# Performance work log

Hardware: AMD Instinct MI355X
Metric: run time of the kernel (lower is better)

Reference implementation:

```python
import jax, jax.numpy as jnp
import numpy as np

B, S, H = 2, 2048, 1024
G, HEADS = 4, 16
HPG = HEADS // G          # heads per group = 4
HD = H // HEADS           # head_dim = 64
DG = H // G               # per-group proj dim = 256
SCALE = 1.0 / np.sqrt(HD)


def setup_inputs() -> dict:
    key = jax.random.key(0)
    ks = jax.random.split(key, 6)
    w = 0.02
    return {
        "hidden_states": jax.random.normal(ks[0], (B, S, H), dtype=jnp.float32),
        "Wq": jax.random.normal(ks[1], (G, DG, H), dtype=jnp.float32) * w,
        "bq": jnp.zeros((G, DG), dtype=jnp.float32),
        "Wk": jax.random.normal(ks[2], (G, DG, H), dtype=jnp.float32) * w,
        "bk": jnp.zeros((G, DG), dtype=jnp.float32),
        "Wv": jax.random.normal(ks[3], (G, DG, H), dtype=jnp.float32) * w,
        "bv": jnp.zeros((G, DG), dtype=jnp.float32),
        "Wo": jax.random.normal(ks[4], (H, H), dtype=jnp.float32) * w,
        "bo": jnp.zeros((H,), dtype=jnp.float32),
    }


def _proj_split(x, W, b):
    # x: [B,S,H], W: [G,DG,H], b: [G,DG] -> [B,G,HPG,S,HD]
    y = jnp.einsum("bsh,gdh->bgsd", x, W) + b[None, :, None, :]
    y = y.reshape(x.shape[0], G, x.shape[1], HPG, HD)
    return jnp.transpose(y, (0, 1, 3, 2, 4))


def reference(hidden_states, Wq, bq, Wk, bk, Wv, bv, Wo, bo):
    q = _proj_split(hidden_states, Wq, bq)  # [B,G,HPG,S,HD]
    k = _proj_split(hidden_states, Wk, bk)
    v = _proj_split(hidden_states, Wv, bv)
    scores = jnp.einsum("bghqd,bghkd->bghqk", q, k) * SCALE
    attn = jax.nn.softmax(scores.astype(jnp.float32), axis=-1).astype(v.dtype)
    ctx = jnp.einsum("bghqk,bghkd->bghqd", attn, v)  # [B,G,HPG,S,HD]
    # merge: heads ordered group-major, matching torch cat over group dim
    ctx = jnp.transpose(ctx, (0, 3, 1, 2, 4)).reshape(hidden_states.shape[0], hidden_states.shape[1], H)
    return jnp.einsum("bsh,oh->bso", ctx, Wo) + bo
```

## Files before the change

### kernel.cpp

```cpp
#include <hip/hip_runtime.h>

typedef __bf16 bf16x8 __attribute__((ext_vector_type(8)));
typedef __bf16 bf16x4 __attribute__((ext_vector_type(4)));
typedef short short4v __attribute__((ext_vector_type(4)));
typedef float f32x4 __attribute__((ext_vector_type(4)));

#define LOG2E 1.4426950408889634f

static __device__ __forceinline__ unsigned short f2bf(float f) {
  union { float f; unsigned int u; } c; c.f = f;
  return (unsigned short)((c.u + 0x7fffu + ((c.u >> 16) & 1u)) >> 16);
}

static __device__ __forceinline__ void gload16(const void* g, void* l) {
  __builtin_amdgcn_global_load_lds(
      (const __attribute__((address_space(1))) void*)g,
      (__attribute__((address_space(3))) void*)l, 16, 0, 0);
}

static __device__ __forceinline__ float expfast(float x) {
#if __has_builtin(__builtin_amdgcn_exp2f)
  return __builtin_amdgcn_exp2f(x * LOG2E);
#else
  return exp2f(x * LOG2E);
#endif
}

#if __has_builtin(__builtin_amdgcn_mfma_f32_16x16x16bf16_1k)
#define MFMA16_FALLBACK 0
static __device__ __forceinline__ f32x4 mfma16(bf16x4 a, bf16x4 b, f32x4 c) {
  return __builtin_amdgcn_mfma_f32_16x16x16bf16_1k(
      __builtin_bit_cast(short4v, a), __builtin_bit_cast(short4v, b), c, 0, 0, 0);
}
#else
#define MFMA16_FALLBACK 1
static __device__ __forceinline__ f32x4 mfma16(bf16x4 a, bf16x4 b, f32x4 c) {
  f32x4 d;
  asm("s_nop 1\n\tv_mfma_f32_16x16x16_bf16 %0, %1, %2, %3"
      : "=v"(d) : "v"(a), "v"(b), "v"(c));
  return d;
}
#endif

__global__ void cvt_all(const float* __restrict__ x,
                        const float* __restrict__ Wq,
                        const float* __restrict__ Wk,
                        const float* __restrict__ Wv,
                        const float* __restrict__ Wo,
                        ushort4* __restrict__ dst) {
  int i = blockIdx.x * 256 + threadIdx.x;
  const float* src;
  int off;
  if (i < 1048576) {
    src = x; off = i;
  } else {
    int t = (i - 1048576) >> 18;
    off = (i - 1048576) & 262143;
    src = (t == 0) ? Wq : (t == 1) ? Wk : (t == 2) ? Wv : Wo;
  }
  float4 f = ((const float4*)src)[off];
  ushort4 o;
  o.x = f2bf(f.x); o.y = f2bf(f.y); o.z = f2bf(f.z); o.w = f2bf(f.w);
  dst[i] = o;
}

__launch_bounds__(256, 2)
__global__ void qkv_gemm(const unsigned short* __restrict__ xb,
                         const unsigned short* __restrict__ wq,
                         const unsigned short* __restrict__ wk,
                         const unsigned short* __restrict__ wv,
                         const float* __restrict__ bq,
                         const float* __restrict__ bk,
                         const float* __restrict__ bv,
                         unsigned short* __restrict__ Qo,
                         unsigned short* __restrict__ Ko,
                         unsigned short* __restrict__ VTo) {
  __shared__ unsigned short As[128 * 64];
  __shared__ unsigned short Bs[128 * 64];
  const int s0 = blockIdx.x * 128;
  const int n0g = blockIdx.y * 128;
  const int qkv = n0g >> 10;
  const int d0 = n0g & 1023;
  const unsigned short* W = (qkv == 0) ? wq : ((qkv == 1) ? wk : wv);
  const float* bias = (qkv == 0) ? bq : ((qkv == 1) ? bk : bv);

  const unsigned short* Aptr; const unsigned short* Bptr;
  int Aoff, Boff;
  if (qkv < 2) { Aptr = W;  Aoff = d0; Bptr = xb; Boff = s0; }
  else         { Aptr = xb; Aoff = s0; Bptr = W;  Boff = d0; }

  const int tid = threadIdx.x;
  const int lane = tid & 63;
  const int wid = tid >> 6;
  const int wm = (wid >> 1) * 64;
  const int wn = (wid & 1) * 64;
  const int lm = lane & 15;
  const int quad = lane >> 4;

  f32x4 acc[4][4] = {};

  for (int kk = 0; kk < 1024; kk += 64) {
#pragma unroll
    for (int t = 0; t < 4; ++t) {
      int i = t * 256 + tid;
      int row = i >> 3, tp = i & 7;
      int seg = tp ^ (row & 7);
      gload16(Aptr + (size_t)(Aoff + row) * 1024 + kk + seg * 8,
              As + (size_t)i * 8);
      gload16(Bptr + (size_t)(Boff + row) * 1024 + kk + seg * 8,
              Bs + (size_t)i * 8);
    }
    __syncthreads();
#pragma unroll
    for (int h = 0; h < 2; ++h) {
      bf16x8 af[4], bff[4];
#pragma unroll
      for (int mt = 0; mt < 4; ++mt) {
        int r = wm + mt * 16 + lm;
        af[mt] = *(const bf16x8*)(As + r * 64 + (((h * 4 + quad) ^ (r & 7)) * 8));
      }
#pragma unroll
      for (int nt = 0; nt < 4; ++nt) {
        int r = wn + nt * 16 + lm;
        bff[nt] = *(const bf16x8*)(Bs + r * 64 + (((h * 4 + quad) ^ (r & 7)) * 8));
      }
#pragma unroll
      for (int mt = 0; mt < 4; ++mt)
#pragma unroll
        for (int nt = 0; nt < 4; ++nt)
          acc[mt][nt] = __builtin_amdgcn_mfma_f32_16x16x32_bf16(
              af[mt], bff[nt], acc[mt][nt], 0, 0, 0);
    }
    __syncthreads();
  }

  if (qkv < 2) {
    unsigned short* OUT = (qkv == 0) ? Qo : Ko;
    const float scale = (qkv == 0) ? 0.125f : 1.0f;
#pragma unroll
    for (int mt = 0; mt < 4; ++mt) {
      const int d = d0 + wm + mt * 16 + quad * 4;
      const int g = d >> 8, hpg = (d >> 6) & 3, hd = d & 63;
      const float4 bb = *(const float4*)(bias + d);
#pragma unroll
      for (int nt = 0; nt < 4; ++nt) {
        const int srow = s0 + wn + nt * 16 + lm;
        const int bidx = srow >> 11, s = srow & 2047;
        const int head = (bidx * 4 + g) * 4 + hpg;
        ushort4 o;
        o.x = f2bf((acc[mt][nt][0] + bb.x) * scale);
        o.y = f2bf((acc[mt][nt][1] + bb.y) * scale);
        o.z = f2bf((acc[mt][nt][2] + bb.z) * scale);
        o.w = f2bf((acc[mt][nt][3] + bb.w) * scale);
        *(ushort4*)(OUT + (size_t)head * 131072 + (size_t)s * 64 + hd) = o;
      }
    }
  } else {
#pragma unroll
    for (int nt = 0; nt < 4; ++nt) {
      const int d = d0 + wn + nt * 16 + lm;
      const int g = d >> 8, hpg = (d >> 6) & 3, hd = d & 63;
      const float bb = bias[d];
#pragma unroll
      for (int mt = 0; mt < 4; ++mt) {
        const int sbase = s0 + wm + mt * 16 + quad * 4;
        const int bidx = sbase >> 11, s = sbase & 2047;
        const int head = (bidx * 4 + g) * 4 + hpg;
        ushort4 o;
        o.x = f2bf(acc[mt][nt][0] + bb);
        o.y = f2bf(acc[mt][nt][1] + bb);
        o.z = f2bf(acc[mt][nt][2] + bb);
        o.w = f2bf(acc[mt][nt][3] + bb);
        *(ushort4*)(VTo + (size_t)head * 131072 + (size_t)hd * 2048 + s) = o;
      }
    }
  }
}

static __device__ __forceinline__ void stage_kv(
    const unsigned short* Kh, const unsigned short* Vh, int kv0,
    unsigned short* ksl, unsigned short* vsl, int tid) {
#pragma unroll
  for (int t = 0; t < 4; ++t) {
    int i = t * 256 + tid;
    int slab = i >> 9, kv = (i >> 2) & 127, tp = i & 3;
    int tc = tp ^ ((kv >> 1) & 3);
    gload16(Kh + (size_t)(kv0 + kv) * 64 + slab * 32 + tc * 8, ksl + (size_t)i * 8);
  }
#pragma unroll
  for (int t = 0; t < 4; ++t) {
    int i = t * 256 + tid;
    int hd = i >> 4, tp = i & 15;
    int tc = tp ^ ((hd >> 1) & 7);
    gload16(Vh + (size_t)hd * 2048 + kv0 + tc * 8, vsl + (size_t)i * 8);
  }
}

__launch_bounds__(256, 2)
__global__ void attn_kernel(const unsigned short* __restrict__ Q,
                            const unsigned short* __restrict__ K,
                            const unsigned short* __restrict__ VT,
                            unsigned short* __restrict__ ctx) {
  __shared__ unsigned short Ks[2][8192];
  __shared__ unsigned short Vs[2][8192];

  const int head = blockIdx.y;
  const int q0 = blockIdx.x * 128;
  const int b = head >> 4;
  const int colbase = (head & 15) * 64;

  const unsigned short* Kh = K + (size_t)head * 131072;
  const unsigned short* Vh = VT + (size_t)head * 131072;

  const int tid = threadIdx.x;
  const int lane = tid & 63;
  const int w = tid >> 6;
  const int lm = lane & 15;
  const int quad = lane >> 4;

  bf16x8 qf[2][2];
#pragma unroll
  for (int nt = 0; nt < 2; ++nt) {
    const size_t qrow = (size_t)(q0 + w * 32 + nt * 16 + lm);
#pragma unroll
    for (int c = 0; c < 2; ++c)
      qf[c][nt] = *(const bf16x8*)(Q + (size_t)head * 131072 + qrow * 64 +
                                   c * 32 + quad * 8);
  }

  stage_kv(Kh, Vh, 0, Ks[0], Vs[0], tid);
  __syncthreads();

  float psum[2] = {0.f, 0.f};
  f32x4 oacc[4][2] = {};
  const int kchunk = (quad ^ ((lm >> 1) & 3)) * 8;

  for (int it = 0; it < 16; ++it) {
    const int buf = it & 1;
    if (it < 15)
      stage_kv(Kh, Vh, (it + 1) * 128, Ks[buf ^ 1], Vs[buf ^ 1], tid);

    const unsigned short* kb = Ks[buf];
    const unsigned short* vb = Vs[buf];

#pragma unroll
    for (int mt = 0; mt < 8; ++mt) {
      f32x4 s0 = {}, s1 = {};
#pragma unroll
      for (int c = 0; c < 2; ++c) {
        bf16x8 kf = *(const bf16x8*)(kb + c * 4096 + (mt * 16 + lm) * 32 + kchunk);
        s0 = __builtin_amdgcn_mfma_f32_16x16x32_bf16(kf, qf[c][0], s0, 0, 0, 0);
        s1 = __builtin_amdgcn_mfma_f32_16x16x32_bf16(kf, qf[c][1], s1, 0, 0, 0);
      }
      bf16x4 pf[2];
#pragma unroll
      for (int nt = 0; nt < 2; ++nt) {
        const f32x4 s = nt ? s1 : s0;
        float e0 = expfast(s[0]), e1 = expfast(s[1]);
        float e2 = expfast(s[2]), e3 = expfast(s[3]);
        psum[nt] += (e0 + e1) + (e2 + e3);
        bf16x4 t;
        t[0] = (__bf16)e0; t[1] = (__bf16)e1; t[2] = (__bf16)e2; t[3] = (__bf16)e3;
        pf[nt] = t;
      }
#pragma unroll
      for (int hm = 0; hm < 4; ++hm) {
        bf16x4 vf = *(const bf16x4*)(vb + (hm * 16 + lm) * 128 +
                                     (((mt * 4 + quad) ^ (lm & 14)) * 4));
        oacc[hm][0] = mfma16(vf, pf[0], oacc[hm][0]);
        oacc[hm][1] = mfma16(vf, pf[1], oacc[hm][1]);
      }
    }
    __syncthreads();
  }

#if MFMA16_FALLBACK
  asm volatile("s_nop 7\n\ts_nop 7");
#endif
#pragma unroll
  for (int nt = 0; nt < 2; ++nt) {
    float p = psum[nt];
    p += __shfl_xor(p, 16, 64);
    p += __shfl_xor(p, 32, 64);
    const float inv = 1.0f / p;
    const size_t row = (size_t)(b * 2048 + q0 + w * 32 + nt * 16 + lm);
#pragma unroll
    for (int hm = 0; hm < 4; ++hm) {
      ushort4 o;
      o.x = f2bf(oacc[hm][nt][0] * inv);
      o.y = f2bf(oacc[hm][nt][1] * inv);
      o.z = f2bf(oacc[hm][nt][2] * inv);
      o.w = f2bf(oacc[hm][nt][3] * inv);
      *(ushort4*)(ctx + row * 1024 + colbase + hm * 16 + quad * 4) = o;
    }
  }
}

__launch_bounds__(256, 4)
__global__ void out_gemm(const unsigned short* __restrict__ A,
                         const unsigned short* __restrict__ Wb,
                         const float* __restrict__ bo,
                         float* __restrict__ out) {
  __shared__ unsigned short As[128 * 64];
  __shared__ unsigned short Bs[64 * 64];
  const int s0 = blockIdx.x * 64;
  const int o0 = blockIdx.y * 128;

  const int tid = threadIdx.x;
  const int lane = tid & 63;
  const int wid = tid >> 6;
  const int wm = (wid >> 1) * 64;
  const int wn = (wid & 1) * 32;
  const int lm = lane & 15;
  const int quad = lane >> 4;

  f32x4 acc[4][2] = {};

  for (int kk = 0; kk < 1024; kk += 64) {
#pragma unroll
    for (int t = 0; t < 4; ++t) {
      int i = t * 256 + tid;
      int row = i >> 3, tp = i & 7;
      int seg = tp ^ (row & 7);
      gload16(Wb + (size_t)(o0 + row) * 1024 + kk + seg * 8, As + (size_t)i * 8);
    }
#pragma unroll
    for (int t = 0; t < 2; ++t) {
      int i = t * 256 + tid;
      int row = i >> 3, tp = i & 7;
      int seg = tp ^ (row & 7);
      gload16(A + (size_t)(s0 + row) * 1024 + kk + seg * 8, Bs + (size_t)i * 8);
    }
    __syncthreads();
#pragma unroll
    for (int h = 0; h < 2; ++h) {
      bf16x8 af[4], bff[2];
#pragma unroll
      for (int mt = 0; mt < 4; ++mt) {
        int r = wm + mt * 16 + lm;
        af[mt] = *(const bf16x8*)(As + r * 64 + (((h * 4 + quad) ^ (r & 7)) * 8));
      }
#pragma unroll
      for (int nt = 0; nt < 2; ++nt) {
        int r = wn + nt * 16 + lm;
        bff[nt] = *(const bf16x8*)(Bs + r * 64 + (((h * 4 + quad) ^ (r & 7)) * 8));
      }
#pragma unroll
      for (int mt = 0; mt < 4; ++mt)
#pragma unroll
        for (int nt = 0; nt < 2; ++nt)
          acc[mt][nt] = __builtin_amdgcn_mfma_f32_16x16x32_bf16(
              af[mt], bff[nt], acc[mt][nt], 0, 0, 0);
    }
    __syncthreads();
  }

#pragma unroll
  for (int mt = 0; mt < 4; ++mt) {
    const int o = o0 + wm + mt * 16 + quad * 4;
    const float4 bb = *(const float4*)(bo + o);
#pragma unroll
    for (int nt = 0; nt < 2; ++nt) {
      const int s = s0 + wn + nt * 16 + lm;
      float4 v;
      v.x = acc[mt][nt][0] + bb.x;
      v.y = acc[mt][nt][1] + bb.y;
      v.z = acc[mt][nt][2] + bb.z;
      v.w = acc[mt][nt][3] + bb.w;
      *(float4*)(out + (size_t)s * 1024 + o) = v;
    }
  }
}

extern "C" void kernel_launch(void* const* d_in, const int* in_sizes, int n_in,
                              void* d_out, int out_size, void* d_ws, size_t ws_size,
                              hipStream_t stream) {
  const float* x  = (const float*)d_in[0];
  const float* Wq = (const float*)d_in[1];
  const float* bq = (const float*)d_in[2];
  const float* Wk = (const float*)d_in[3];
  const float* bk = (const float*)d_in[4];
  const float* Wv = (const float*)d_in[5];
  const float* bv = (const float*)d_in[6];
  const float* Wo = (const float*)d_in[7];
  const float* bo = (const float*)d_in[8];
  float* out = (float*)d_out;

  char* ws = (char*)d_ws;
  unsigned short* xb  = (unsigned short*)(ws + 0);
  unsigned short* wqb = (unsigned short*)(ws + 8388608);
  unsigned short* wkb = (unsigned short*)(ws + 10485760);
  unsigned short* wvb = (unsigned short*)(ws + 12582912);
  unsigned short* wob = (unsigned short*)(ws + 14680064);
  unsigned short* Qb  = (unsigned short*)(ws + 16777216);
  unsigned short* Kb  = (unsigned short*)(ws + 25165824);
  unsigned short* VTb = (unsigned short*)(ws + 33554432);
  unsigned short* ctxb= (unsigned short*)(ws + 41943040);
  if (ws_size < 50331648) return;

  cvt_all<<<8192, 256, 0, stream>>>(x, Wq, Wk, Wv, Wo, (ushort4*)ws);
  qkv_gemm<<<dim3(32, 24), 256, 0, stream>>>(xb, wqb, wkb, wvb, bq, bk, bv,
                                             Qb, Kb, VTb);
  attn_kernel<<<dim3(16, 32), 256, 0, stream>>>(Qb, Kb, VTb, ctxb);
  out_gemm<<<dim3(64, 8), 256, 0, stream>>>(ctxb, wob, bo, out);
}
```

Baseline: 197.0 us.

## Split attention KV tile across wave pairs and fold log2e into Q scale

```diff
diff --git a/kernel.cpp b/kernel.cpp
--- a/kernel.cpp
+++ b/kernel.cpp
@@ -18,11 +18,11 @@
       (__attribute__((address_space(3))) void*)l, 16, 0, 0);
 }
 
-static __device__ __forceinline__ float expfast(float x) {
+static __device__ __forceinline__ float exp2fast(float x) {
 #if __has_builtin(__builtin_amdgcn_exp2f)
-  return __builtin_amdgcn_exp2f(x * LOG2E);
+  return __builtin_amdgcn_exp2f(x);
 #else
-  return exp2f(x * LOG2E);
+  return exp2f(x);
 #endif
 }
 
@@ -136,7 +136,7 @@
 
   if (qkv < 2) {
     unsigned short* OUT = (qkv == 0) ? Qo : Ko;
-    const float scale = (qkv == 0) ? 0.125f : 1.0f;
+    const float scale = (qkv == 0) ? (0.125f * LOG2E) : 1.0f;
 #pragma unroll
     for (int mt = 0; mt < 4; ++mt) {
       const int d = d0 + wm + mt * 16 + quad * 4;
@@ -201,8 +201,7 @@
                             const unsigned short* __restrict__ K,
                             const unsigned short* __restrict__ VT,
                             unsigned short* __restrict__ ctx) {
-  __shared__ unsigned short Ks[2][8192];
-  __shared__ unsigned short Vs[2][8192];
+  __shared__ __align__(16) unsigned char smem[65536];
 
   const int head = blockIdx.y;
   const int q0 = blockIdx.x * 128;
@@ -215,60 +214,67 @@
   const int tid = threadIdx.x;
   const int lane = tid & 63;
   const int w = tid >> 6;
+  const int wq = w & 1;
+  const int wkv = w >> 1;
   const int lm = lane & 15;
   const int quad = lane >> 4;
 
-  bf16x8 qf[2][2];
-#pragma unroll
-  for (int nt = 0; nt < 2; ++nt) {
-    const size_t qrow = (size_t)(q0 + w * 32 + nt * 16 + lm);
+  bf16x8 qf[2][4];
+#pragma unroll
+  for (int nt = 0; nt < 4; ++nt) {
+    const size_t qrow = (size_t)(q0 + wq * 64 + nt * 16 + lm);
 #pragma unroll
     for (int c = 0; c < 2; ++c)
       qf[c][nt] = *(const bf16x8*)(Q + (size_t)head * 131072 + qrow * 64 +
                                    c * 32 + quad * 8);
   }
 
-  stage_kv(Kh, Vh, 0, Ks[0], Vs[0], tid);
+  stage_kv(Kh, Vh, 0, (unsigned short*)smem,
+           (unsigned short*)(smem + 32768), tid);
   __syncthreads();
 
-  float psum[2] = {0.f, 0.f};
-  f32x4 oacc[4][2] = {};
+  float psum[4] = {0.f, 0.f, 0.f, 0.f};
+  f32x4 oacc[4][4] = {};
   const int kchunk = (quad ^ ((lm >> 1) & 3)) * 8;
 
   for (int it = 0; it < 16; ++it) {
     const int buf = it & 1;
+    const unsigned short* kb = (const unsigned short*)(smem + buf * 16384);
+    const unsigned short* vb = (const unsigned short*)(smem + 32768 + buf * 16384);
     if (it < 15)
-      stage_kv(Kh, Vh, (it + 1) * 128, Ks[buf ^ 1], Vs[buf ^ 1], tid);
-
-    const unsigned short* kb = Ks[buf];
-    const unsigned short* vb = Vs[buf];
-
-#pragma unroll
-    for (int mt = 0; mt < 8; ++mt) {
-      f32x4 s0 = {}, s1 = {};
+      stage_kv(Kh, Vh, (it + 1) * 128,
+               (unsigned short*)(smem + (buf ^ 1) * 16384),
+               (unsigned short*)(smem + 32768 + (buf ^ 1) * 16384), tid);
+
+#pragma unroll
+    for (int mt = 0; mt < 4; ++mt) {
+      const int kvrow = wkv * 64 + mt * 16 + lm;
+      f32x4 s[4] = {};
 #pragma unroll
       for (int c = 0; c < 2; ++c) {
-        bf16x8 kf = *(const bf16x8*)(kb + c * 4096 + (mt * 16 + lm) * 32 + kchunk);
-        s0 = __builtin_amdgcn_mfma_f32_16x16x32_bf16(kf, qf[c][0], s0, 0, 0, 0);
-        s1 = __builtin_amdgcn_mfma_f32_16x16x32_bf16(kf, qf[c][1], s1, 0, 0, 0);
-      }
-      bf16x4 pf[2];
-#pragma unroll
-      for (int nt = 0; nt < 2; ++nt) {
-        const f32x4 s = nt ? s1 : s0;
-        float e0 = expfast(s[0]), e1 = expfast(s[1]);
-        float e2 = expfast(s[2]), e3 = expfast(s[3]);
+        bf16x8 kf = *(const bf16x8*)(kb + c * 4096 + kvrow * 32 + kchunk);
+#pragma unroll
+        for (int nt = 0; nt < 4; ++nt)
+          s[nt] = __builtin_amdgcn_mfma_f32_16x16x32_bf16(kf, qf[c][nt], s[nt],
+                                                          0, 0, 0);
+      }
+      bf16x4 pf[4];
+#pragma unroll
+      for (int nt = 0; nt < 4; ++nt) {
+        float e0 = exp2fast(s[nt][0]), e1 = exp2fast(s[nt][1]);
+        float e2 = exp2fast(s[nt][2]), e3 = exp2fast(s[nt][3]);
         psum[nt] += (e0 + e1) + (e2 + e3);
         bf16x4 t;
         t[0] = (__bf16)e0; t[1] = (__bf16)e1; t[2] = (__bf16)e2; t[3] = (__bf16)e3;
         pf[nt] = t;
       }
+      const int vgran = ((wkv * 16 + mt * 4 + quad) ^ (lm & 14)) * 4;
 #pragma unroll
       for (int hm = 0; hm < 4; ++hm) {
-        bf16x4 vf = *(const bf16x4*)(vb + (hm * 16 + lm) * 128 +
-                                     (((mt * 4 + quad) ^ (lm & 14)) * 4));
-        oacc[hm][0] = mfma16(vf, pf[0], oacc[hm][0]);
-        oacc[hm][1] = mfma16(vf, pf[1], oacc[hm][1]);
+        bf16x4 vf = *(const bf16x4*)(vb + (hm * 16 + lm) * 128 + vgran);
+#pragma unroll
+        for (int nt = 0; nt < 4; ++nt)
+          oacc[hm][nt] = mfma16(vf, pf[nt], oacc[hm][nt]);
       }
     }
     __syncthreads();
@@ -278,20 +284,41 @@
   asm volatile("s_nop 7\n\ts_nop 7");
 #endif
 #pragma unroll
-  for (int nt = 0; nt < 2; ++nt) {
-    float p = psum[nt];
-    p += __shfl_xor(p, 16, 64);
-    p += __shfl_xor(p, 32, 64);
-    const float inv = 1.0f / p;
-    const size_t row = (size_t)(b * 2048 + q0 + w * 32 + nt * 16 + lm);
-#pragma unroll
-    for (int hm = 0; hm < 4; ++hm) {
-      ushort4 o;
-      o.x = f2bf(oacc[hm][nt][0] * inv);
-      o.y = f2bf(oacc[hm][nt][1] * inv);
-      o.z = f2bf(oacc[hm][nt][2] * inv);
-      o.w = f2bf(oacc[hm][nt][3] * inv);
-      *(ushort4*)(ctx + row * 1024 + colbase + hm * 16 + quad * 4) = o;
+  for (int nt = 0; nt < 4; ++nt) {
+    psum[nt] += __shfl_xor(psum[nt], 16, 64);
+    psum[nt] += __shfl_xor(psum[nt], 32, 64);
+  }
+
+  float* red = (float*)smem;
+  float* psred = (float*)(smem + 34816);
+  if (wkv == 1) {
+#pragma unroll
+    for (int nt = 0; nt < 4; ++nt) {
+      const int qi = wq * 64 + nt * 16 + lm;
+      if (quad == 0) psred[qi] = psum[nt];
+#pragma unroll
+      for (int hm = 0; hm < 4; ++hm)
+        *(f32x4*)(red + qi * 68 + hm * 16 + quad * 4) = oacc[hm][nt];
+    }
+  }
+  __syncthreads();
+  if (wkv == 0) {
+#pragma unroll
+    for (int nt = 0; nt < 4; ++nt) {
+      const int qi = wq * 64 + nt * 16 + lm;
+      const float inv = 1.0f / (psum[nt] + psred[qi]);
+      const size_t row = (size_t)(b * 2048 + q0 + qi);
+#pragma unroll
+      for (int hm = 0; hm < 4; ++hm) {
+        f32x4 o = *(const f32x4*)(red + qi * 68 + hm * 16 + quad * 4);
+        o += oacc[hm][nt];
+        ushort4 st;
+        st.x = f2bf(o[0] * inv);
+        st.y = f2bf(o[1] * inv);
+        st.z = f2bf(o[2] * inv);
+        st.w = f2bf(o[3] * inv);
+        *(ushort4*)(ctx + row * 1024 + colbase + hm * 16 + quad * 4) = st;
+      }
     }
   }
 }
```

After: 182.4 us. 7.4% less time.
